# Performance work log

Measured on AMD Instinct MI355X. Metric: run time of the kernel, lower is better.

The kernel has to match this reference:

```python
import jax, jax.numpy as jnp
import numpy as np

N_FEATURES = 170
D_MODEL = 64
N_HEADS = 4
ALPHA = 0.1
LN_EPS = 1e-5
LEAKY_SLOPE = 0.01  # torch F.leaky_relu default
N = 3 * N_FEATURES  # 510
B = 32


def setup_inputs() -> dict:
    key = jax.random.key(0)
    ks = jax.random.split(key, 10)
    D, H = D_MODEL, N_HEADS
    s = 1.0 / np.sqrt(D)
    return {
        "x": jax.random.normal(ks[0], (B, N, D), dtype=jnp.float32),
        "causal_graph": jax.random.uniform(ks[1], (N, N), dtype=jnp.float32),
        # nn.Linear(d_model, d_model*n_heads, bias=False): stored here as (D, H*D) for x @ W
        "W": jax.random.uniform(ks[2], (D, H * D), jnp.float32, -s, s),
        "attention_w": jax.random.normal(ks[3], (H, 2 * D), dtype=jnp.float32),
        # Conv2d(2, n_heads, 3, padding=1): OIHW kernel
        "conv_w": jax.random.uniform(ks[4], (H, 2, 3, 3), jnp.float32, -1/np.sqrt(18), 1/np.sqrt(18)),
        "conv_b": jax.random.uniform(ks[5], (H,), jnp.float32, -1/np.sqrt(18), 1/np.sqrt(18)),
        # nn.Linear(d_model, 2*d_model): stored as (D, 2D)
        "fcg_w": jax.random.uniform(ks[6], (D, 2 * D), jnp.float32, -s, s),
        "fcg_b": jax.random.uniform(ks[7], (2 * D,), jnp.float32, -s, s),
        "ln_g": jnp.ones((D,), jnp.float32),
        "ln_b": jnp.zeros((D,), jnp.float32),
    }


def reference(x, causal_graph, W, attention_w, conv_w, conv_b, fcg_w, fcg_b, ln_g, ln_b):
    Bz, Nn, D = x.shape
    H = N_HEADS
    # shared projection: (B, N, H, D)
    xt = (x @ W).reshape(Bz, Nn, H, D)
    # GAT-style additive scores: concat-dot decomposed into two dot products
    w1, w2 = attention_w[:, :D], attention_w[:, D:]  # each (H, D)
    s_i = jnp.einsum('bnhd,hd->bhn', xt, w1)  # source term
    s_j = jnp.einsum('bnhd,hd->bhn', xt, w2)  # target term
    e = s_i[:, :, :, None] + s_j[:, :, None, :]  # (B, H, N, N)
    A_eva = jnp.where(e >= 0, e, LEAKY_SLOPE * e)  # leaky_relu
    # fuse mean attention with causal graph via 3x3 conv
    A_mean = A_eva.mean(axis=1)  # (B, N, N)
    causal = jnp.broadcast_to(causal_graph[None], (Bz, Nn, Nn))
    stacked = jnp.stack([A_mean, causal], axis=1)  # (B, 2, N, N)
    A_st = jax.lax.conv_general_dilated(
        stacked, conv_w, window_strides=(1, 1), padding=((1, 1), (1, 1)),
        dimension_numbers=('NCHW', 'OIHW', 'NCHW'))
    A_st = A_st + conv_b[None, :, None, None]  # (B, H, N, N)
    A = jax.nn.softmax(ALPHA * A_eva + (1.0 - ALPHA) * A_st, axis=-1)
    # multi-head aggregation then head-mean
    out = jnp.einsum('bhnm,bmhd->bnhd', A, xt).mean(axis=2)  # (B, N, D)
    # GLU
    g = out @ fcg_w + fcg_b  # (B, N, 2D)
    a, b = g[..., :D], g[..., D:]
    glu = a * jax.nn.sigmoid(b)
    # residual + layernorm
    y = glu + x
    mu = y.mean(axis=-1, keepdims=True)
    var = ((y - mu) ** 2).mean(axis=-1, keepdims=True)
    y = (y - mu) * jax.lax.rsqrt(var + LN_EPS) * ln_g + ln_b
    return y, A
```

## Files before the change

kernel.cpp:

```cpp
#include <hip/hip_runtime.h>

#define Bz 32
#define Nn 510
#define Dd 64
#define Hh 4
#define HD_ 256
#define Kpad 512
#define ALPHA_ 0.1f
#define LNEPS 1e-5f
#define SLOPE 0.01f
#define NEG_INF -3.0e38f

typedef __attribute__((ext_vector_type(8))) short short8;
typedef __attribute__((ext_vector_type(4))) float floatx4;

__device__ inline float wredsum(float v) {
  #pragma unroll
  for (int off = 32; off; off >>= 1) v += __shfl_xor(v, off, 64);
  return v;
}
__device__ inline float wredmax(float v) {
  #pragma unroll
  for (int off = 32; off; off >>= 1) v = fmaxf(v, __shfl_xor(v, off, 64));
  return v;
}
__device__ inline unsigned short f2bf(float f) {
  unsigned int u = __float_as_uint(f);
  unsigned int r = (u + 0x7fffu + ((u >> 16) & 1u)) >> 16;
  return (unsigned short)r;
}

__global__ __launch_bounds__(256) void k1_xt(const float* __restrict__ x,
                                             const float* __restrict__ W,
                                             const float* __restrict__ attw,
                                             unsigned short* __restrict__ xtT,
                                             float* __restrict__ si,
                                             float* __restrict__ sj) {
  __shared__ float Wl[64][68];
  __shared__ float xr[32][68];
  __shared__ unsigned short st[64 * 33];
  const int t = threadIdx.x;
  const int rt = blockIdx.x;
  const int b = blockIdx.y;
  const int ch = blockIdx.z;
  #pragma unroll
  for (int k = 0; k < 4; k++) {
    int f = t + k * 256;
    int kr = f >> 4;
    int c = (f & 15) * 4;
    *(float4*)&Wl[kr][c] = *(const float4*)&W[kr * HD_ + ch * 64 + c];
  }
  #pragma unroll
  for (int k = 0; k < 2; k++) {
    int f = t + k * 256;
    int r = f >> 4;
    int c = (f & 15) * 4;
    int row = rt * 32 + r;
    float4 v = make_float4(0.f, 0.f, 0.f, 0.f);
    if (row < Nn) v = *(const float4*)&x[(b * Nn + row) * Dd + c];
    *(float4*)&xr[r][c] = v;
  }
  __syncthreads();
  const int tg = t >> 4;
  const int tc = t & 15;
  const int rb = tg * 2, c0 = tc * 4;
  float acc[2][4] = {};
  #pragma unroll
  for (int k4 = 0; k4 < 16; k4++) {
    float4 xv0 = *(float4*)&xr[rb][k4 * 4];
    float4 xv1 = *(float4*)&xr[rb + 1][k4 * 4];
    #pragma unroll
    for (int kk = 0; kk < 4; kk++) {
      float4 wv = *(float4*)&Wl[k4 * 4 + kk][c0];
      float xs0 = (&xv0.x)[kk];
      float xs1 = (&xv1.x)[kk];
      acc[0][0] = fmaf(xs0, wv.x, acc[0][0]);
      acc[0][1] = fmaf(xs0, wv.y, acc[0][1]);
      acc[0][2] = fmaf(xs0, wv.z, acc[0][2]);
      acc[0][3] = fmaf(xs0, wv.w, acc[0][3]);
      acc[1][0] = fmaf(xs1, wv.x, acc[1][0]);
      acc[1][1] = fmaf(xs1, wv.y, acc[1][1]);
      acc[1][2] = fmaf(xs1, wv.z, acc[1][2]);
      acc[1][3] = fmaf(xs1, wv.w, acc[1][3]);
    }
  }
  #pragma unroll
  for (int cc = 0; cc < 4; cc++) {
    #pragma unroll
    for (int r = 0; r < 2; r++) {
      st[(c0 + cc) * 33 + rb + r] = f2bf(acc[r][cc]);
    }
  }
  float w1v[4], w2v[4];
  #pragma unroll
  for (int cc = 0; cc < 4; cc++) {
    w1v[cc] = attw[ch * 128 + c0 + cc];
    w2v[cc] = attw[ch * 128 + 64 + c0 + cc];
  }
  #pragma unroll
  for (int r = 0; r < 2; r++) {
    float p1 = acc[r][0] * w1v[0] + acc[r][1] * w1v[1] +
               acc[r][2] * w1v[2] + acc[r][3] * w1v[3];
    float p2 = acc[r][0] * w2v[0] + acc[r][1] * w2v[1] +
               acc[r][2] * w2v[2] + acc[r][3] * w2v[3];
    #pragma unroll
    for (int off = 1; off <= 8; off <<= 1) {
      p1 += __shfl_xor(p1, off, 64);
      p2 += __shfl_xor(p2, off, 64);
    }
    if (tc == 0) {
      int row = rt * 32 + rb + r;
      if (row < Nn) {
        si[(b * 4 + ch) * Nn + row] = p1;
        sj[(b * 4 + ch) * Nn + row] = p2;
      }
    }
  }
  __syncthreads();
  if (t < 64) {
    unsigned short* dst = &xtT[((size_t)(b * 4 + ch) * 64 + t) * Kpad + rt * 32];
    #pragma unroll
    for (int q = 0; q < 4; q++) {
      short8 v;
      #pragma unroll
      for (int k = 0; k < 8; k++) v[k] = (short)st[t * 33 + q * 8 + k];
      *(short8*)&dst[q * 8] = v;
    }
  }
}

__global__ __launch_bounds__(256) void k2a_cconv(const float* __restrict__ causal,
                                                 const float* __restrict__ convw,
                                                 const float* __restrict__ convb,
                                                 float* __restrict__ ccv) {
  const int i = blockIdx.x;
  const int t = threadIdx.x;
  #pragma unroll
  for (int qq = 0; qq < 2; qq++) {
    const int j = t + qq * 256;
    float tap[9];
    #pragma unroll
    for (int r3 = 0; r3 < 3; r3++) {
      int ii = i - 1 + r3;
      #pragma unroll
      for (int c3 = 0; c3 < 3; c3++) {
        int jj = j - 1 + c3;
        tap[r3 * 3 + c3] = (ii >= 0 && ii < Nn && jj >= 0 && jj < Nn)
                               ? causal[ii * Nn + jj] : 0.f;
      }
    }
    #pragma unroll
    for (int h = 0; h < 4; h++) {
      float acc = convb[h];
      #pragma unroll
      for (int q = 0; q < 9; q++) acc = fmaf(convw[h * 18 + 9 + q], tap[q], acc);
      ccv[((size_t)h * Nn + i) * 512 + j] = acc;
    }
  }
}

__global__ __launch_bounds__(256) void k2_attn(const float* __restrict__ si,
                                               const float* __restrict__ sj,
                                               const float* __restrict__ ccv,
                                               const float* __restrict__ convw,
                                               float* __restrict__ A) {
  __shared__ float am_t[10 * 8 * 68];
  __shared__ float sjl[4 * 8 * 68];
  __shared__ float sil[4][12];
  __shared__ float cwl[4][9];
  const int t = threadIdx.x;
  const int i0 = blockIdx.x * 8;
  const int b = blockIdx.y;
  if (t < 36) cwl[t / 9][t % 9] = convw[(t / 9) * 18 + (t % 9)];
  if (t < 40) {
    int h = t / 10, r = t % 10;
    int iq = i0 + r - 1;
    sil[h][r] = (iq >= 0 && iq < Nn) ? si[(b * 4 + h) * Nn + iq] : 0.f;
  }
  if (t >= 64 && t < 224) {
    int q = t - 64;
    int r = q >> 4, rem = q & 15;
    int e = rem >> 1, side = rem & 1;
    am_t[(r * 8 + e) * 68 + side * 65] = 0.f;
  }
  for (int f = t; f < 2048; f += 256) {
    int h = f >> 9, j = f & 511;
    float v = (j < Nn) ? sj[(b * 4 + h) * Nn + j] : 0.f;
    sjl[(h * 8 + (j & 7)) * 68 + (j >> 3) + 1] = v;
  }
  __syncthreads();
  for (int f = t; f < 5120; f += 256) {
    int r = f >> 9, j = f & 511;
    int iq = i0 + r - 1;
    float am = 0.f;
    if (iq >= 0 && iq < Nn && j < Nn) {
      float s = 0.f;
      #pragma unroll
      for (int h = 0; h < 4; h++) {
        float e2 = sil[h][r] + sjl[(h * 8 + (j & 7)) * 68 + (j >> 3) + 1];
        s += (e2 >= 0.f) ? e2 : SLOPE * e2;
      }
      am = 0.25f * s;
    }
    am_t[(r * 8 + (j & 7)) * 68 + (j >> 3) + 1] = am;
  }
  __syncthreads();
  const int w = t >> 6, L = t & 63;
  const int j0 = L * 8;
  #pragma unroll
  for (int qq = 0; qq < 2; qq++) {
    const int il = w * 2 + qq;
    const int i = i0 + il;
    if (i >= Nn) continue;
    float conv[4][8];
    #pragma unroll
    for (int h = 0; h < 4; h++) {
      const float* cp = &ccv[((size_t)h * Nn + i) * 512 + j0];
      float4 c0 = *(const float4*)&cp[0];
      float4 c1 = *(const float4*)&cp[4];
      conv[h][0] = c0.x; conv[h][1] = c0.y; conv[h][2] = c0.z; conv[h][3] = c0.w;
      conv[h][4] = c1.x; conv[h][5] = c1.y; conv[h][6] = c1.z; conv[h][7] = c1.w;
    }
    #pragma unroll
    for (int r3 = 0; r3 < 3; r3++) {
      const float* ba = &am_t[((il + r3) * 8) * 68];
      float a[10];
      a[0] = ba[7 * 68 + L];
      #pragma unroll
      for (int e = 0; e < 8; e++) a[1 + e] = ba[e * 68 + L + 1];
      a[9] = ba[0 * 68 + L + 2];
      #pragma unroll
      for (int h = 0; h < 4; h++) {
        float w0 = cwl[h][r3 * 3], w1 = cwl[h][r3 * 3 + 1], w2 = cwl[h][r3 * 3 + 2];
        #pragma unroll
        for (int e = 0; e < 8; e++) {
          float cv = conv[h][e];
          cv = fmaf(w0, a[e], cv);
          cv = fmaf(w1, a[e + 1], cv);
          cv = fmaf(w2, a[e + 2], cv);
          conv[h][e] = cv;
        }
      }
    }
    #pragma unroll
    for (int h = 0; h < 4; h++) {
      const float sih = sil[h][il + 1];
      float v[8];
      float mx = NEG_INF;
      #pragma unroll
      for (int e = 0; e < 8; e++) {
        float ee = sih + sjl[(h * 8 + e) * 68 + L + 1];
        float l = (ee >= 0.f) ? ee : SLOPE * ee;
        float val = ALPHA_ * l + (1.0f - ALPHA_) * conv[h][e];
        v[e] = (j0 + e < Nn) ? val : NEG_INF;
        mx = fmaxf(mx, v[e]);
      }
      mx = wredmax(mx);
      float p[8], s = 0.f;
      #pragma unroll
      for (int e = 0; e < 8; e++) {
        p[e] = __expf(v[e] - mx);
        s += p[e];
      }
      s = wredsum(s);
      const float inv = 1.f / s;
      #pragma unroll
      for (int e = 0; e < 8; e++) p[e] *= inv;
      float* Ar = &A[((size_t)(b * 4 + h) * Nn + i) * Nn + j0];
      *(float4*)&Ar[0] = make_float4(p[0], p[1], p[2], p[3]);
      if (L < 63) {
        *(float4*)&Ar[4] = make_float4(p[4], p[5], p[6], p[7]);
      } else {
        *(float2*)&Ar[4] = make_float2(p[4], p[5]);
      }
    }
  }
}

__global__ __launch_bounds__(256) void k3_out(const float* __restrict__ A,
                                              const unsigned short* __restrict__ xtT,
                                              const float* __restrict__ x,
                                              const float* __restrict__ fcgw,
                                              const float* __restrict__ fcgb,
                                              const float* __restrict__ lng,
                                              const float* __restrict__ lnb,
                                              float* __restrict__ y) {
  __shared__ unsigned short Asub[3][16 * 72];
  __shared__ float ol[16][64];
  __shared__ float gl[2][128];
  const int t = threadIdx.x;
  const int n0 = blockIdx.x * 16;
  const int b = blockIdx.y;
  const int w = t >> 6, L = t & 63;
  const int quad = L >> 4, l16 = L & 15;
  const int wc = w * 16;
  const int ar = t >> 4;
  const int amc = (t & 15) * 4;
  const int nrow = n0 + ar;
  floatx4 acc = {0.f, 0.f, 0.f, 0.f};

  auto loadA = [&](int p, float* av) {
    const int h = p >> 3;
    const int m = (p & 7) * 64 + amc;
    av[0] = av[1] = av[2] = av[3] = 0.f;
    if (nrow < Nn) {
      const float* src = &A[((size_t)(b * 4 + h) * Nn + nrow) * Nn + m];
      if (m + 3 < Nn) {
        float2 v0 = *(const float2*)&src[0];
        float2 v1 = *(const float2*)&src[2];
        av[0] = v0.x; av[1] = v0.y; av[2] = v1.x; av[3] = v1.y;
      } else {
        int lim = Nn - m;
        #pragma unroll
        for (int q = 0; q < 4; q++) if (q < lim) av[q] = src[q];
      }
    }
  };
  auto writeA = [&](int p, const float* av) {
    ushort4 u;
    u.x = f2bf(av[0]); u.y = f2bf(av[1]);
    u.z = f2bf(av[2]); u.w = f2bf(av[3]);
    *(ushort4*)&Asub[p % 3][ar * 72 + amc] = u;
  };

  float rvA[4], rvB[4];
  loadA(0, rvA);
  loadA(1, rvB);
  writeA(0, rvA);
  __syncthreads();
  #pragma unroll
  for (int p = 0; p < 32; p++) {
    if (p + 2 < 32) loadA(p + 2, (p & 1) ? rvB : rvA);
    if (p + 1 < 32) writeA(p + 1, (p & 1) ? rvA : rvB);
    __syncthreads();
    const int h = p >> 3;
    const unsigned short* Xr =
        &xtT[((size_t)(b * 4 + h) * 64 + wc + l16) * Kpad + (p & 7) * 64];
    const unsigned short* Ab = &Asub[p % 3][l16 * 72];
    short8 af0 = *(const short8*)&Ab[quad * 8];
    short8 bf0 = *(const short8*)&Xr[quad * 8];
    acc = __builtin_amdgcn_mfma_f32_16x16x32_bf16(af0, bf0, acc, 0, 0, 0);
    short8 af1 = *(const short8*)&Ab[32 + quad * 8];
    short8 bf1 = *(const short8*)&Xr[32 + quad * 8];
    acc = __builtin_amdgcn_mfma_f32_16x16x32_bf16(af1, bf1, acc, 0, 0, 0);
  }

  __syncthreads();
  #pragma unroll
  for (int reg = 0; reg < 4; reg++) {
    ol[quad * 4 + reg][wc + l16] = 0.25f * acc[reg];
  }
  __syncthreads();
  const int kk = t & 127;
  const int rg = t >> 7;
  for (int it = 0; it < 8; it++) {
    const int r = it * 2 + rg;
    const int row = n0 + r;
    float g = fcgb[kk];
    #pragma unroll
    for (int d = 0; d < 64; d++) g = fmaf(ol[r][d], fcgw[d * 128 + kk], g);
    gl[rg][kk] = g;
    __syncthreads();
    if (kk < 64 && row < Nn) {
      float a = gl[rg][kk];
      float bb = gl[rg][kk + 64];
      float glu = a / (1.f + __expf(-bb));
      float yv = glu + x[(b * Nn + row) * Dd + kk];
      float mu = wredsum(yv) * (1.f / 64.f);
      float dv = yv - mu;
      float var = wredsum(dv * dv) * (1.f / 64.f);
      float o = dv * rsqrtf(var + LNEPS) * lng[kk] + lnb[kk];
      y[(b * Nn + row) * Dd + kk] = o;
    }
    __syncthreads();
  }
}

extern "C" void kernel_launch(void* const* d_in, const int* in_sizes, int n_in,
                              void* d_out, int out_size, void* d_ws, size_t ws_size,
                              hipStream_t stream) {
  const float* x      = (const float*)d_in[0];
  const float* causal = (const float*)d_in[1];
  const float* W      = (const float*)d_in[2];
  const float* attw   = (const float*)d_in[3];
  const float* convw  = (const float*)d_in[4];
  const float* convb  = (const float*)d_in[5];
  const float* fcgw   = (const float*)d_in[6];
  const float* fcgb   = (const float*)d_in[7];
  const float* lng    = (const float*)d_in[8];
  const float* lnb    = (const float*)d_in[9];

  float* ws = (float*)d_ws;
  float* si = ws;
  float* sj = si + (size_t)Bz * Hh * Nn;
  unsigned short* xtT = (unsigned short*)(sj + (size_t)Bz * Hh * Nn + 16);
  float* ccv = (float*)(xtT + (size_t)Bz * Hh * Dd * Kpad);

  float* yout = (float*)d_out;
  float* Aout = yout + (size_t)Bz * Nn * Dd;

  k2a_cconv<<<dim3(Nn), 256, 0, stream>>>(causal, convw, convb, ccv);
  k1_xt  <<<dim3(16, Bz, 4), 256, 0, stream>>>(x, W, attw, xtT, si, sj);
  k2_attn<<<dim3(64, Bz), 256, 0, stream>>>(si, sj, ccv, convw, Aout);
  k3_out <<<dim3(32, Bz), 256, 0, stream>>>(Aout, xtT, x, fcgw, fcgb, lng, lnb, yout);
}
```

Baseline: 260.1 us.

## Emit bf16 copy of attention matrix and consume it in aggregation kernel

The attention kernel now also writes a padded bf16 copy of A into workspace, and a new aggregation kernel reads it directly with MFMA instead of re-reading and converting the fp32 A output. This halves the bytes read in the aggregation stage and drops the shared-memory staging, at the cost of an extra 64MB-class write in the attention kernel. The path depends on the workspace being large enough, and otherwise falls back to the old kernel.

```diff
diff --git a/kernel.cpp b/kernel.cpp
--- a/kernel.cpp
+++ b/kernel.cpp
@@ -163,7 +163,8 @@
                                                const float* __restrict__ sj,
                                                const float* __restrict__ ccv,
                                                const float* __restrict__ convw,
-                                               float* __restrict__ A) {
+                                               float* __restrict__ A,
+                                               unsigned short* __restrict__ a16) {
   __shared__ float am_t[10 * 8 * 68];
   __shared__ float sjl[4 * 8 * 68];
   __shared__ float sil[4][12];
@@ -273,7 +274,76 @@
       } else {
         *(float2*)&Ar[4] = make_float2(p[4], p[5]);
       }
-    }
+      if (a16) {
+        short8 pv;
+        #pragma unroll
+        for (int e = 0; e < 8; e++) pv[e] = (short)f2bf(p[e]);
+        *(short8*)&a16[(((size_t)(b * 4 + h) * 512 + i) * 512) + j0] = pv;
+      }
+    }
+  }
+}
+
+__global__ __launch_bounds__(256) void k3_a16(const unsigned short* __restrict__ A16,
+                                              const unsigned short* __restrict__ xtT,
+                                              const float* __restrict__ x,
+                                              const float* __restrict__ fcgw,
+                                              const float* __restrict__ fcgb,
+                                              const float* __restrict__ lng,
+                                              const float* __restrict__ lnb,
+                                              float* __restrict__ y) {
+  __shared__ float ol[16][64];
+  __shared__ float gl[2][128];
+  const int t = threadIdx.x;
+  const int n0 = blockIdx.x * 16;
+  const int b = blockIdx.y;
+  const int w = t >> 6, L = t & 63;
+  const int quad = L >> 4, l16 = L & 15;
+  const int wc = w * 16;
+  const int arow = (n0 + l16 < Nn) ? (n0 + l16) : (Nn - 1);
+  floatx4 acc = {0.f, 0.f, 0.f, 0.f};
+  #pragma unroll
+  for (int h = 0; h < 4; h++) {
+    const unsigned short* Ar = &A16[(((size_t)(b * 4 + h) * 512) + arow) * 512];
+    const unsigned short* Xr = &xtT[((size_t)(b * 4 + h) * 64 + wc + l16) * Kpad];
+    #pragma unroll
+    for (int kt = 0; kt < 8; kt++) {
+      const int m = kt * 64;
+      short8 af0 = *(const short8*)&Ar[m + quad * 8];
+      short8 bf0 = *(const short8*)&Xr[m + quad * 8];
+      acc = __builtin_amdgcn_mfma_f32_16x16x32_bf16(af0, bf0, acc, 0, 0, 0);
+      short8 af1 = *(const short8*)&Ar[m + 32 + quad * 8];
+      short8 bf1 = *(const short8*)&Xr[m + 32 + quad * 8];
+      acc = __builtin_amdgcn_mfma_f32_16x16x32_bf16(af1, bf1, acc, 0, 0, 0);
+    }
+  }
+  #pragma unroll
+  for (int reg = 0; reg < 4; reg++) {
+    ol[quad * 4 + reg][wc + l16] = 0.25f * acc[reg];
+  }
+  __syncthreads();
+  const int kk = t & 127;
+  const int rg = t >> 7;
+  for (int it = 0; it < 8; it++) {
+    const int r = it * 2 + rg;
+    const int row = n0 + r;
+    float g = fcgb[kk];
+    #pragma unroll
+    for (int d = 0; d < 64; d++) g = fmaf(ol[r][d], fcgw[d * 128 + kk], g);
+    gl[rg][kk] = g;
+    __syncthreads();
+    if (kk < 64 && row < Nn) {
+      float a = gl[rg][kk];
+      float bb = gl[rg][kk + 64];
+      float glu = a / (1.f + __expf(-bb));
+      float yv = glu + x[(b * Nn + row) * Dd + kk];
+      float mu = wredsum(yv) * (1.f / 64.f);
+      float dv = yv - mu;
+      float var = wredsum(dv * dv) * (1.f / 64.f);
+      float o = dv * rsqrtf(var + LNEPS) * lng[kk] + lnb[kk];
+      y[(b * Nn + row) * Dd + kk] = o;
+    }
+    __syncthreads();
   }
 }
 
@@ -396,11 +466,21 @@
   unsigned short* xtT = (unsigned short*)(sj + (size_t)Bz * Hh * Nn + 16);
   float* ccv = (float*)(xtT + (size_t)Bz * Hh * Dd * Kpad);
 
+  const size_t base_bytes = 13088832;
+  const size_t a16_bytes  = (size_t)Bz * Hh * 512 * 512 * 2;
+  const bool use16 = ws_size >= base_bytes + a16_bytes;
+  unsigned short* a16 =
+      use16 ? (unsigned short*)((char*)d_ws + base_bytes) : (unsigned short*)0;
+
   float* yout = (float*)d_out;
   float* Aout = yout + (size_t)Bz * Nn * Dd;
 
   k2a_cconv<<<dim3(Nn), 256, 0, stream>>>(causal, convw, convb, ccv);
   k1_xt  <<<dim3(16, Bz, 4), 256, 0, stream>>>(x, W, attw, xtT, si, sj);
-  k2_attn<<<dim3(64, Bz), 256, 0, stream>>>(si, sj, ccv, convw, Aout);
-  k3_out <<<dim3(32, Bz), 256, 0, stream>>>(Aout, xtT, x, fcgw, fcgb, lng, lnb, yout);
-}
+  k2_attn<<<dim3(64, Bz), 256, 0, stream>>>(si, sj, ccv, convw, Aout, a16);
+  if (use16) {
+    k3_a16<<<dim3(32, Bz), 256, 0, stream>>>(a16, xtT, x, fcgw, fcgb, lng, lnb, yout);
+  } else {
+    k3_out<<<dim3(32, Bz), 256, 0, stream>>>(Aout, xtT, x, fcgw, fcgb, lng, lnb, yout);
+  }
+}
```

Result: slower. 283.7 us (+9.1%).
